# Optimization experiments

Hardware: AMD Instinct MI355X
Metric: run time of the kernel (lower is better)

## Reference

```python
import jax, jax.numpy as jnp
import numpy as np

INPUT_SIZE = 512
OUTPUT_SIZE = 512
BATCH = 65536
HIDDEN = [256, 128, 64, 32]


def _linear_params(key, fan_in, fan_out):
    # torch nn.Linear default init: U(-1/sqrt(fan_in), 1/sqrt(fan_in))
    kw, kb = jax.random.split(key)
    bound = 1.0 / np.sqrt(fan_in)
    w = jax.random.uniform(kw, (fan_out, fan_in), jnp.float32, -bound, bound)
    b = jax.random.uniform(kb, (fan_out,), jnp.float32, -bound, bound)
    return w, b


def setup_inputs() -> dict:
    key = jax.random.key(0)
    ks = jax.random.split(key, 6)
    x = jax.random.normal(ks[0], (BATCH, INPUT_SIZE), jnp.float32)
    dims = [INPUT_SIZE] + HIDDEN + [OUTPUT_SIZE]
    inp = {"x": x}
    for i in range(5):
        w, b = _linear_params(ks[i + 1], dims[i], dims[i + 1])
        inp[f"w{i+1}"] = w
        inp[f"b{i+1}"] = b
    return inp


def reference(x, w1, b1, w2, b2, w3, b3, w4, b4, w5, b5):
    sig = jax.nn.sigmoid
    # in_size = number of nonzero entries in row 0 (replaces per-element python loop)
    in_size = jnp.count_nonzero(x[0])  # traced int scalar
    h = sig(x @ w1.T + b1)
    h = sig(h @ w2.T + b2)
    h = sig(h @ w3.T + b3)
    h = sig(h @ w4.T + b4)
    y = h @ w5.T + b5  # [B, OUTPUT_SIZE]
    # out has shape [B, INPUT_SIZE]; out[:, :in_size] = y[:, :in_size]
    # (INPUT_SIZE == OUTPUT_SIZE here, so a prefix mask suffices)
    mask = jnp.arange(INPUT_SIZE) < in_size  # [INPUT_SIZE]
    out = jnp.where(mask[None, :], y, jnp.zeros((), y.dtype))
    return out
```

## Files before the change

### kernel.cpp

```cpp
#include <hip/hip_runtime.h>
#include <hip/hip_bf16.h>
#include <stdint.h>

typedef __attribute__((ext_vector_type(4))) float f32x4;
typedef __attribute__((ext_vector_type(4))) unsigned int u32x4;
typedef __attribute__((ext_vector_type(8))) short short8;

#define MFMA16(a, b, c) __builtin_amdgcn_mfma_f32_16x16x32_bf16((a), (b), (c), 0, 0, 0)

__device__ __forceinline__ uint16_t f2bf(float f) {
  __hip_bfloat16 h = __float2bfloat16(f);
  return __builtin_bit_cast(uint16_t, h);
}

__device__ __forceinline__ float fast_sigmoid(float v) {
  return __builtin_amdgcn_rcpf(1.f + __expf(-v));
}

__device__ __forceinline__ short8 cvt8(f32x4 a, f32x4 b) {
  short8 r;
  r[0] = (short)f2bf(a[0]); r[1] = (short)f2bf(a[1]);
  r[2] = (short)f2bf(a[2]); r[3] = (short)f2bf(a[3]);
  r[4] = (short)f2bf(b[0]); r[5] = (short)f2bf(b[1]);
  r[6] = (short)f2bf(b[2]); r[7] = (short)f2bf(b[3]);
  return r;
}

template <int RB>
__device__ __forceinline__ int swzoff(int row, int bcol) {
  constexpr int SLM = (((RB / 16) < 8 ? (RB / 16) : 8)) - 1;
  return row * RB + (bcol ^ ((row & SLM) << 4));
}

template <int RB>
__device__ __forceinline__ short8 lds_a(const uint16_t* buf, int row0, int k0, int lane) {
  int r = row0 + (lane & 15);
  int bcol = (k0 + ((lane >> 4) << 3)) * 2;
  u32x4 raw = *(const u32x4*)((const char*)buf + swzoff<RB>(r, bcol));
  return __builtin_bit_cast(short8, raw);
}

__device__ __forceinline__ short8 lds_a_s(const char* sb, int row0, int lane) {
  int r = row0 + (lane & 15);
  return *(const short8*)(sb + r * 80 + ((lane >> 4) << 4));
}

__device__ __forceinline__ short8 load_frag_f32(const float* M, int ld, int r0, int k0, int lane) {
  const float* p = M + (size_t)(r0 + (lane & 15)) * ld + (k0 + ((lane >> 4) << 3));
  f32x4 a = *(const f32x4*)p;
  f32x4 b = *(const f32x4*)(p + 4);
  return cvt8(a, b);
}

__device__ __forceinline__ short8 load_b_pk(const char* base, int f, int lane) {
  u32x4 raw = *(const u32x4*)(base + (((size_t)f * 64 + lane) << 4));
  return __builtin_bit_cast(short8, raw);
}

template <bool P>
__device__ __forceinline__ short8 bfrag(const char* wp, const float* W, int K,
                                        int f0, int ntg, int KT, int kt, int lane) {
  if constexpr (P) {
    return load_b_pk(wp, f0 + ntg * KT + kt, lane);
  } else {
    return load_frag_f32(W, K, ntg * 16, kt * 32, lane);
  }
}

__global__ void pack_kernel(const float* __restrict__ w1, const float* __restrict__ w2,
                            const float* __restrict__ w3, const float* __restrict__ w4,
                            const float* __restrict__ w5, char* __restrict__ ws) {
  int b = blockIdx.x, lane = threadIdx.x;
  const float* W;
  int K, f0;
  if (b < 256)      { W = w1; K = 512; f0 = 0; }
  else if (b < 320) { W = w2; K = 256; f0 = 256; }
  else if (b < 336) { W = w3; K = 128; f0 = 320; }
  else if (b < 340) { W = w4; K = 64;  f0 = 336; }
  else              { W = w5; K = 32;  f0 = 340; }
  int f = b - f0;
  int KT = K / 32;
  int nt = f / KT, kt = f % KT;
  short8 r = load_frag_f32(W, K, nt * 16, kt * 32, lane);
  *(u32x4*)(ws + (((size_t)b * 64 + lane) << 4)) = __builtin_bit_cast(u32x4, r);
}

#define CHUNK_BAR()                                           \
  asm volatile("s_waitcnt lgkmcnt(0)" ::: "memory");          \
  __builtin_amdgcn_s_barrier();                               \
  __builtin_amdgcn_sched_barrier(0);

#define KSTEP(C)                                                              \
  {                                                                           \
    CHUNK_BAR();                                                              \
    if ((C) + 2 < 16) {                                                       \
      const float* p = xrow + ((C) + 2) * 32;                                 \
      rA[(C) & 1][0] = *(const f32x4*)p;                                      \
      rA[(C) & 1][1] = *(const f32x4*)(p + 4);                                \
    }                                                                         \
    if ((C) + 1 < 16) {                                                       \
      _Pragma("unroll") for (int nt = 0; nt < 4; ++nt)                        \
          bfr[((C) + 1) & 1][nt] =                                            \
              bfrag<P>(wp, w1, 512, 0, wid * 4 + nt, 16, (C) + 1, lane);      \
    }                                                                         \
    __builtin_amdgcn_sched_barrier(0);                                        \
    if ((C) + 1 < 16) {                                                       \
      short8 wv = cvt8(rA[((C) + 1) & 1][0], rA[((C) + 1) & 1][1]);           \
      *(short8*)(sring + (((C) + 1) & 1) * 5120 + swb) = wv;                  \
    }                                                                         \
    const char* sc = sring + ((C) & 1) * 5120;                                \
    _Pragma("unroll") for (int m = 0; m < 4; ++m) {                           \
      short8 a = lds_a_s(sc, m * 16, lane);                                   \
      _Pragma("unroll") for (int nt = 0; nt < 4; ++nt)                        \
          acc[m][nt] = MFMA16(a, bfr[(C) & 1][nt], acc[m][nt]);               \
    }                                                                         \
  }

template <bool P>
__global__ __launch_bounds__(256, 3) void mlp5_kernel(
    const float* __restrict__ x,
    const float* __restrict__ w1, const float* __restrict__ b1,
    const float* __restrict__ w2, const float* __restrict__ b2,
    const float* __restrict__ w3, const float* __restrict__ b3,
    const float* __restrict__ w4, const float* __restrict__ b4,
    const float* __restrict__ w5, const float* __restrict__ b5,
    const char* __restrict__ wp, float* __restrict__ out) {
  __shared__ __align__(16) char smem[32 * 1024];
  uint16_t* H1 = (uint16_t*)smem;
  uint16_t* H2 = (uint16_t*)smem;
  uint16_t* H3 = (uint16_t*)(smem + 16 * 1024);
  uint16_t* H4 = (uint16_t*)(smem + 24 * 1024);

  const int tid = threadIdx.x;
  const int lane = tid & 63;
  const int wid = tid >> 6;
  const int row0 = blockIdx.x * 64;
  const int lr = (lane >> 4) << 2;
  const int lc = lane & 15;

  int in_size = 0;
#pragma unroll
  for (int j = 0; j < 8; ++j) {
    float v = x[j * 64 + lane];
    in_size += (int)__popcll(__ballot(v != 0.f));
  }

  char* sring = smem;
  const float* xrow =
      x + (size_t)(row0 + wid * 16 + (lane & 15)) * 512 + ((lane >> 4) << 3);
  const int swb = (wid * 16 + (lane & 15)) * 80 + ((lane >> 4) << 4);

  f32x4 acc[4][4];
#pragma unroll
  for (int m = 0; m < 4; ++m)
#pragma unroll
    for (int n = 0; n < 4; ++n) acc[m][n] = (f32x4){0.f, 0.f, 0.f, 0.f};

  f32x4 rA[2][2];
  short8 bfr[2][4];
  rA[0][0] = *(const f32x4*)(xrow + 0);
  rA[0][1] = *(const f32x4*)(xrow + 4);
  rA[1][0] = *(const f32x4*)(xrow + 32);
  rA[1][1] = *(const f32x4*)(xrow + 36);
#pragma unroll
  for (int nt = 0; nt < 4; ++nt)
    bfr[0][nt] = bfrag<P>(wp, w1, 512, 0, wid * 4 + nt, 16, 0, lane);
  {
    short8 wv = cvt8(rA[0][0], rA[0][1]);
    *(short8*)(sring + swb) = wv;
  }

  KSTEP(0)  KSTEP(1)  KSTEP(2)  KSTEP(3)
  KSTEP(4)  KSTEP(5)  KSTEP(6)  KSTEP(7)
  KSTEP(8)  KSTEP(9)  KSTEP(10) KSTEP(11)
  KSTEP(12) KSTEP(13) KSTEP(14) KSTEP(15)

  short8 bfr2[2][8];
#pragma unroll
  for (int n = 0; n < 2; ++n)
#pragma unroll
    for (int kt = 0; kt < 8; ++kt)
      bfr2[n][kt] = bfrag<P>(wp, w2, 256, 256, wid * 2 + n, 8, kt, lane);

  __syncthreads();

#pragma unroll
  for (int n = 0; n < 4; ++n) {
    const int ncol = wid * 64 + n * 16;
    const float bv = b1[ncol + lc];
#pragma unroll
    for (int m = 0; m < 4; ++m)
#pragma unroll
      for (int i = 0; i < 4; ++i) {
        float v = fast_sigmoid(acc[m][n][i] + bv);
        *(uint16_t*)((char*)H1 + swzoff<512>(m * 16 + lr + i, (ncol + lc) * 2)) = f2bf(v);
      }
  }
  __syncthreads();

  {
    f32x4 acc2[4][2];
#pragma unroll
    for (int m = 0; m < 4; ++m)
#pragma unroll
      for (int n = 0; n < 2; ++n) acc2[m][n] = (f32x4){0.f, 0.f, 0.f, 0.f};
#pragma unroll
    for (int m = 0; m < 4; ++m) {
#pragma unroll
      for (int kt = 0; kt < 8; ++kt) {
        short8 afr = lds_a<512>(H1, m * 16, kt * 32, lane);
        acc2[m][0] = MFMA16(afr, bfr2[0][kt], acc2[m][0]);
        acc2[m][1] = MFMA16(afr, bfr2[1][kt], acc2[m][1]);
      }
    }
    short8 bfr3[4];
#pragma unroll
    for (int kt = 0; kt < 4; ++kt)
      bfr3[kt] = bfrag<P>(wp, w3, 128, 320, wid, 4, kt, lane);
    __syncthreads();
#pragma unroll
    for (int n = 0; n < 2; ++n) {
      const int ncol = wid * 32 + n * 16;
      const float bv = b2[ncol + lc];
#pragma unroll
      for (int m = 0; m < 4; ++m)
#pragma unroll
        for (int i = 0; i < 4; ++i) {
          float v = fast_sigmoid(acc2[m][n][i] + bv);
          *(uint16_t*)((char*)H2 + swzoff<256>(m * 16 + lr + i, (ncol + lc) * 2)) = f2bf(v);
        }
    }
    __syncthreads();

    f32x4 acc3[4];
#pragma unroll
    for (int m = 0; m < 4; ++m) acc3[m] = (f32x4){0.f, 0.f, 0.f, 0.f};
#pragma unroll
    for (int m = 0; m < 4; ++m)
#pragma unroll
      for (int kt = 0; kt < 4; ++kt) {
        short8 afr = lds_a<256>(H2, m * 16, kt * 32, lane);
        acc3[m] = MFMA16(afr, bfr3[kt], acc3[m]);
      }
    short8 bfr4[2];
#pragma unroll
    for (int kt = 0; kt < 2; ++kt)
      bfr4[kt] = bfrag<P>(wp, w4, 64, 336, wid & 1, 2, kt, lane);
    {
      const int ncol = wid * 16;
      const float bv = b3[ncol + lc];
#pragma unroll
      for (int m = 0; m < 4; ++m)
#pragma unroll
        for (int i = 0; i < 4; ++i) {
          float v = fast_sigmoid(acc3[m][i] + bv);
          *(uint16_t*)((char*)H3 + swzoff<128>(m * 16 + lr + i, (ncol + lc) * 2)) = f2bf(v);
        }
    }
    __syncthreads();

    const int wm = wid >> 1, wn = wid & 1;
    f32x4 acc4[2];
#pragma unroll
    for (int mt = 0; mt < 2; ++mt) acc4[mt] = (f32x4){0.f, 0.f, 0.f, 0.f};
#pragma unroll
    for (int mt = 0; mt < 2; ++mt)
#pragma unroll
      for (int kt = 0; kt < 2; ++kt) {
        short8 afr = lds_a<128>(H3, wm * 32 + mt * 16, kt * 32, lane);
        acc4[mt] = MFMA16(afr, bfr4[kt], acc4[mt]);
      }
    short8 bfr5[8];
#pragma unroll
    for (int nt = 0; nt < 8; ++nt)
      bfr5[nt] = bfrag<P>(wp, w5, 32, 340, wid * 8 + nt, 1, 0, lane);
    {
      const int ncol = wn * 16;
      const float bv = b4[ncol + lc];
#pragma unroll
      for (int mt = 0; mt < 2; ++mt)
#pragma unroll
        for (int i = 0; i < 4; ++i) {
          float v = fast_sigmoid(acc4[mt][i] + bv);
          *(uint16_t*)((char*)H4 + swzoff<64>(wm * 32 + mt * 16 + lr + i, (ncol + lc) * 2)) = f2bf(v);
        }
    }
    __syncthreads();

#pragma unroll
    for (int m = 0; m < 4; ++m) {
      short8 afr = lds_a<64>(H4, m * 16, 0, lane);
#pragma unroll
      for (int nt = 0; nt < 8; ++nt) {
        f32x4 av = MFMA16(afr, bfr5[nt], ((f32x4){0.f, 0.f, 0.f, 0.f}));
        const int col = wid * 128 + nt * 16 + lc;
        const float bv = b5[col];
        const bool keep = col < in_size;
#pragma unroll
        for (int i = 0; i < 4; ++i) {
          float v = keep ? (av[i] + bv) : 0.f;
          out[(size_t)(row0 + m * 16 + lr + i) * 512 + col] = v;
        }
      }
    }
  }
}

extern "C" void kernel_launch(void* const* d_in, const int* in_sizes, int n_in,
                              void* d_out, int out_size, void* d_ws, size_t ws_size,
                              hipStream_t stream) {
  const float* x  = (const float*)d_in[0];
  const float* w1 = (const float*)d_in[1];
  const float* b1 = (const float*)d_in[2];
  const float* w2 = (const float*)d_in[3];
  const float* b2 = (const float*)d_in[4];
  const float* w3 = (const float*)d_in[5];
  const float* b3 = (const float*)d_in[6];
  const float* w4 = (const float*)d_in[7];
  const float* b4 = (const float*)d_in[8];
  const float* w5 = (const float*)d_in[9];
  const float* b5 = (const float*)d_in[10];
  float* out = (float*)d_out;

  dim3 grid(65536 / 64);
  dim3 block(256);
  const bool packed = ws_size >= (size_t)(372 * 1024);
  if (packed) {
    pack_kernel<<<372, 64, 0, stream>>>(w1, w2, w3, w4, w5, (char*)d_ws);
    mlp5_kernel<true><<<grid, block, 0, stream>>>(x, w1, b1, w2, b2, w3, b3, w4, b4,
                                                  w5, b5, (const char*)d_ws, out);
  } else {
    mlp5_kernel<false><<<grid, block, 0, stream>>>(x, w1, b1, w2, b2, w3, b3, w4, b4,
                                                   w5, b5, nullptr, out);
  }
}
```

Baseline: 78.66 us.

## Double K-chunk size in layer-1 pipeline and hoist bias loads before barriers

The layer-1 loop now stages 64-wide K chunks per barrier instead of 32, halving the number of LDS barrier round-trips. It uses a 144-byte padded row stride and interleaves the weight-fragment reloads between the two half-chunk MFMA groups. Bias loads for all layers are hoisted ahead of barriers so their global latency overlaps other work. The cost is more registers for the prefetched x tiles and larger LDS staging, which at launch bounds of 3 blocks per CU may cause spills.

```diff
diff --git a/kernel.cpp b/kernel.cpp
--- a/kernel.cpp
+++ b/kernel.cpp
@@ -40,9 +40,9 @@
   return __builtin_bit_cast(short8, raw);
 }
 
-__device__ __forceinline__ short8 lds_a_s(const char* sb, int row0, int lane) {
+__device__ __forceinline__ short8 lds_a144(const char* sb, int row0, int kk, int lane) {
   int r = row0 + (lane & 15);
-  return *(const short8*)(sb + r * 80 + ((lane >> 4) << 4));
+  return *(const short8*)(sb + r * 144 + ((kk * 4 + (lane >> 4)) << 4));
 }
 
 __device__ __forceinline__ short8 load_frag_f32(const float* M, int ld, int r0, int k0, int lane) {
@@ -90,29 +90,43 @@
   __builtin_amdgcn_s_barrier();                               \
   __builtin_amdgcn_sched_barrier(0);
 
-#define KSTEP(C)                                                              \
+#define KSTEP64(C)                                                            \
   {                                                                           \
     CHUNK_BAR();                                                              \
-    if ((C) + 2 < 16) {                                                       \
-      const float* p = xrow + ((C) + 2) * 32;                                 \
+    if ((C) + 2 < 8) {                                                        \
+      const float* p = xrow + ((C) + 2) * 64;                                 \
       rA[(C) & 1][0] = *(const f32x4*)p;                                      \
       rA[(C) & 1][1] = *(const f32x4*)(p + 4);                                \
-    }                                                                         \
-    if ((C) + 1 < 16) {                                                       \
+      rA[(C) & 1][2] = *(const f32x4*)(p + 32);                               \
+      rA[(C) & 1][3] = *(const f32x4*)(p + 36);                               \
+    }                                                                         \
+    if ((C) + 1 < 8) {                                                        \
+      short8 wv0 = cvt8(rA[((C) + 1) & 1][0], rA[((C) + 1) & 1][1]);          \
+      short8 wv1 = cvt8(rA[((C) + 1) & 1][2], rA[((C) + 1) & 1][3]);          \
+      char* wb = sring + (((C) + 1) & 1) * 9216 + swb;                        \
+      *(short8*)(wb) = wv0;                                                   \
+      *(short8*)(wb + 64) = wv1;                                              \
+    }                                                                         \
+    const char* sc = sring + ((C) & 1) * 9216;                                \
+    _Pragma("unroll") for (int m = 0; m < 4; ++m) {                           \
+      short8 a = lds_a144(sc, m * 16, 0, lane);                               \
       _Pragma("unroll") for (int nt = 0; nt < 4; ++nt)                        \
-          bfr[((C) + 1) & 1][nt] =                                            \
-              bfrag<P>(wp, w1, 512, 0, wid * 4 + nt, 16, (C) + 1, lane);      \
-    }                                                                         \
-    __builtin_amdgcn_sched_barrier(0);                                        \
-    if ((C) + 1 < 16) {                                                       \
-      short8 wv = cvt8(rA[((C) + 1) & 1][0], rA[((C) + 1) & 1][1]);           \
-      *(short8*)(sring + (((C) + 1) & 1) * 5120 + swb) = wv;                  \
-    }                                                                         \
-    const char* sc = sring + ((C) & 1) * 5120;                                \
+          acc[m][nt] = MFMA16(a, bfr[0][nt], acc[m][nt]);                     \
+    }                                                                         \
+    if (2 * (C) + 2 < 16) {                                                   \
+      _Pragma("unroll") for (int nt = 0; nt < 4; ++nt)                        \
+          bfr[0][nt] =                                                        \
+              bfrag<P>(wp, w1, 512, 0, wid * 4 + nt, 16, 2 * (C) + 2, lane);  \
+    }                                                                         \
     _Pragma("unroll") for (int m = 0; m < 4; ++m) {                           \
-      short8 a = lds_a_s(sc, m * 16, lane);                                   \
+      short8 a = lds_a144(sc, m * 16, 1, lane);                               \
       _Pragma("unroll") for (int nt = 0; nt < 4; ++nt)                        \
-          acc[m][nt] = MFMA16(a, bfr[(C) & 1][nt], acc[m][nt]);               \
+          acc[m][nt] = MFMA16(a, bfr[1][nt], acc[m][nt]);                     \
+    }                                                                         \
+    if (2 * (C) + 3 < 16) {                                                   \
+      _Pragma("unroll") for (int nt = 0; nt < 4; ++nt)                        \
+          bfr[1][nt] =                                                        \
+              bfrag<P>(wp, w1, 512, 0, wid * 4 + nt, 16, 2 * (C) + 3, lane);  \
     }                                                                         \
   }
 
@@ -148,7 +162,7 @@
   char* sring = smem;
   const float* xrow =
       x + (size_t)(row0 + wid * 16 + (lane & 15)) * 512 + ((lane >> 4) << 3);
-  const int swb = (wid * 16 + (lane & 15)) * 80 + ((lane >> 4) << 4);
+  const int swb = (wid * 16 + (lane & 15)) * 144 + ((lane >> 4) << 4);
 
   f32x4 acc[4][4];
 #pragma unroll
@@ -156,24 +170,31 @@
 #pragma unroll
     for (int n = 0; n < 4; ++n) acc[m][n] = (f32x4){0.f, 0.f, 0.f, 0.f};
 
-  f32x4 rA[2][2];
+  f32x4 rA[2][4];
   short8 bfr[2][4];
   rA[0][0] = *(const f32x4*)(xrow + 0);
   rA[0][1] = *(const f32x4*)(xrow + 4);
-  rA[1][0] = *(const f32x4*)(xrow + 32);
-  rA[1][1] = *(const f32x4*)(xrow + 36);
+  rA[0][2] = *(const f32x4*)(xrow + 32);
+  rA[0][3] = *(const f32x4*)(xrow + 36);
+  rA[1][0] = *(const f32x4*)(xrow + 64);
+  rA[1][1] = *(const f32x4*)(xrow + 68);
+  rA[1][2] = *(const f32x4*)(xrow + 96);
+  rA[1][3] = *(const f32x4*)(xrow + 100);
 #pragma unroll
   for (int nt = 0; nt < 4; ++nt)
     bfr[0][nt] = bfrag<P>(wp, w1, 512, 0, wid * 4 + nt, 16, 0, lane);
+#pragma unroll
+  for (int nt = 0; nt < 4; ++nt)
+    bfr[1][nt] = bfrag<P>(wp, w1, 512, 0, wid * 4 + nt, 16, 1, lane);
   {
-    short8 wv = cvt8(rA[0][0], rA[0][1]);
-    *(short8*)(sring + swb) = wv;
-  }
-
-  KSTEP(0)  KSTEP(1)  KSTEP(2)  KSTEP(3)
-  KSTEP(4)  KSTEP(5)  KSTEP(6)  KSTEP(7)
-  KSTEP(8)  KSTEP(9)  KSTEP(10) KSTEP(11)
-  KSTEP(12) KSTEP(13) KSTEP(14) KSTEP(15)
+    short8 wv0 = cvt8(rA[0][0], rA[0][1]);
+    short8 wv1 = cvt8(rA[0][2], rA[0][3]);
+    *(short8*)(sring + swb) = wv0;
+    *(short8*)(sring + swb + 64) = wv1;
+  }
+
+  KSTEP64(0) KSTEP64(1) KSTEP64(2) KSTEP64(3)
+  KSTEP64(4) KSTEP64(5) KSTEP64(6) KSTEP64(7)
 
   short8 bfr2[2][8];
 #pragma unroll
@@ -181,18 +202,20 @@
 #pragma unroll
     for (int kt = 0; kt < 8; ++kt)
       bfr2[n][kt] = bfrag<P>(wp, w2, 256, 256, wid * 2 + n, 8, kt, lane);
+  float bv1[4];
+#pragma unroll
+  for (int n = 0; n < 4; ++n) bv1[n] = b1[wid * 64 + n * 16 + lc];
 
   __syncthreads();
 
 #pragma unroll
   for (int n = 0; n < 4; ++n) {
     const int ncol = wid * 64 + n * 16;
-    const float bv = b1[ncol + lc];
 #pragma unroll
     for (int m = 0; m < 4; ++m)
 #pragma unroll
       for (int i = 0; i < 4; ++i) {
-        float v = fast_sigmoid(acc[m][n][i] + bv);
+        float v = fast_sigmoid(acc[m][n][i] + bv1[n]);
         *(uint16_t*)((char*)H1 + swzoff<512>(m * 16 + lr + i, (ncol + lc) * 2)) = f2bf(v);
       }
   }
@@ -217,16 +240,18 @@
 #pragma unroll
     for (int kt = 0; kt < 4; ++kt)
       bfr3[kt] = bfrag<P>(wp, w3, 128, 320, wid, 4, kt, lane);
+    float bv2[2];
+#pragma unroll
+    for (int n = 0; n < 2; ++n) bv2[n] = b2[wid * 32 + n * 16 + lc];
     __syncthreads();
 #pragma unroll
     for (int n = 0; n < 2; ++n) {
       const int ncol = wid * 32 + n * 16;
-      const float bv = b2[ncol + lc];
 #pragma unroll
       for (int m = 0; m < 4; ++m)
 #pragma unroll
         for (int i = 0; i < 4; ++i) {
-          float v = fast_sigmoid(acc2[m][n][i] + bv);
+          float v = fast_sigmoid(acc2[m][n][i] + bv2[n]);
           *(uint16_t*)((char*)H2 + swzoff<256>(m * 16 + lr + i, (ncol + lc) * 2)) = f2bf(v);
         }
     }
@@ -246,15 +271,14 @@
 #pragma unroll
     for (int kt = 0; kt < 2; ++kt)
       bfr4[kt] = bfrag<P>(wp, w4, 64, 336, wid & 1, 2, kt, lane);
+    const float bv3 = b3[wid * 16 + lc];
     {
-      const int ncol = wid * 16;
-      const float bv = b3[ncol + lc];
 #pragma unroll
       for (int m = 0; m < 4; ++m)
 #pragma unroll
         for (int i = 0; i < 4; ++i) {
-          float v = fast_sigmoid(acc3[m][i] + bv);
-          *(uint16_t*)((char*)H3 + swzoff<128>(m * 16 + lr + i, (ncol + lc) * 2)) = f2bf(v);
+          float v = fast_sigmoid(acc3[m][i] + bv3);
+          *(uint16_t*)((char*)H3 + swzoff<128>(m * 16 + lr + i, (wid * 16 + lc) * 2)) = f2bf(v);
         }
     }
     __syncthreads();
@@ -274,15 +298,17 @@
 #pragma unroll
     for (int nt = 0; nt < 8; ++nt)
       bfr5[nt] = bfrag<P>(wp, w5, 32, 340, wid * 8 + nt, 1, 0, lane);
+    const float bv4 = b4[wn * 16 + lc];
+    float bv5[8];
+#pragma unroll
+    for (int nt = 0; nt < 8; ++nt) bv5[nt] = b5[wid * 128 + nt * 16 + lc];
     {
-      const int ncol = wn * 16;
-      const float bv = b4[ncol + lc];
 #pragma unroll
       for (int mt = 0; mt < 2; ++mt)
 #pragma unroll
         for (int i = 0; i < 4; ++i) {
-          float v = fast_sigmoid(acc4[mt][i] + bv);
-          *(uint16_t*)((char*)H4 + swzoff<64>(wm * 32 + mt * 16 + lr + i, (ncol + lc) * 2)) = f2bf(v);
+          float v = fast_sigmoid(acc4[mt][i] + bv4);
+          *(uint16_t*)((char*)H4 + swzoff<64>(wm * 32 + mt * 16 + lr + i, (wn * 16 + lc) * 2)) = f2bf(v);
         }
     }
     __syncthreads();
@@ -294,11 +320,10 @@
       for (int nt = 0; nt < 8; ++nt) {
         f32x4 av = MFMA16(afr, bfr5[nt], ((f32x4){0.f, 0.f, 0.f, 0.f}));
         const int col = wid * 128 + nt * 16 + lc;
-        const float bv = b5[col];
         const bool keep = col < in_size;
 #pragma unroll
         for (int i = 0; i < 4; ++i) {
-          float v = keep ? (av[i] + bv) : 0.f;
+          float v = keep ? (av[i] + bv5[nt]) : 0.f;
           out[(size_t)(row0 + m * 16 + lr + i) * 512 + col] = v;
         }
       }
```

Measured after the change: 76.15 us. 3.2% less time.
